# Optimization experiments

Hardware: AMD Instinct MI355X
Metric: run time of the kernel (lower is better)

Reference implementation:

```python
import jax, jax.numpy as jnp
import numpy as np

NUM_CLASSES = 91
NUM_ANCHORS = 3234
VAR_XY, VAR_WH = 0.1, 0.2
SCORE_THRESH = 0.05
NMS_THRESH = 0.5
PRE_NMS_TOPK = 200  # original default 400; reduced to bound the [C-1,K,K] IoU buffer
MAX_DET = 100
BATCH = 64


def _xyxy_to_cxcywh(b):
    wh = b[..., 2:] - b[..., :2]
    c = b[..., :2] + 0.5 * wh
    return jnp.concatenate([c, wh], axis=-1)


def _pairwise_iou(b):
    # b: [K,4] xyxy -> [K,K] IoU
    lt = jnp.maximum(b[:, None, :2], b[None, :, :2])
    rb = jnp.minimum(b[:, None, 2:], b[None, :, 2:])
    inter = jnp.prod(jnp.clip(rb - lt, 0.0), axis=-1)
    area = jnp.prod(jnp.clip(b[:, 2:] - b[:, :2], 0.0), axis=-1)
    union = area[:, None] + area[None, :] - inter
    return inter / jnp.maximum(union, 1e-9)


def _nms_keep(boxes):
    # boxes [K,4] already sorted by descending score; greedy NMS keep mask [K]
    K = boxes.shape[0]
    iou = _pairwise_iou(jax.lax.stop_gradient(boxes))
    idx = jnp.arange(K)

    def body(i, keep):
        suppress = keep[i] & (iou[i] > NMS_THRESH) & (idx > i)
        return keep & ~suppress

    return jax.lax.fori_loop(0, K, body, jnp.ones((K,), dtype=bool))


def setup_inputs() -> dict:
    key = jax.random.key(0)
    k1, k2, k3, k4 = jax.random.split(key, 4)
    cls_logits = jax.random.normal(k1, (BATCH, NUM_ANCHORS, NUM_CLASSES), dtype=jnp.float32)
    box_reg = jax.random.normal(k2, (BATCH, NUM_ANCHORS, 4), dtype=jnp.float32)
    # valid normalized anchor boxes in xyxy
    cxy = jax.random.uniform(k3, (NUM_ANCHORS, 2), minval=0.05, maxval=0.95)
    wh = jax.random.uniform(k4, (NUM_ANCHORS, 2), minval=0.02, maxval=0.4)
    priors = jnp.concatenate([cxy - wh / 2, cxy + wh / 2], axis=-1).astype(jnp.float32)
    return {"cls_logits": cls_logits, "box_reg": box_reg, "priors": priors}


def reference(cls_logits, box_reg, priors):
    probs = jax.nn.softmax(cls_logits, axis=-1)           # [B,A,C]
    pr_c = _xyxy_to_cxcywh(priors)                        # [A,4]

    def per_image(args):
        loc, p = args                                     # [A,4], [A,C]
        # _decode with variances (0.1, 0.2)
        xy = loc[:, :2] * VAR_XY * pr_c[:, 2:] + pr_c[:, :2]
        wh = jnp.exp(loc[:, 2:] * VAR_WH) * pr_c[:, 2:]
        boxes = jnp.concatenate([xy - wh / 2, xy + wh / 2], axis=-1)  # [A,4]

        scores_c = p[:, 1:].T                             # [C-1, A], skip background
        vals, idx = jax.lax.top_k(scores_c, PRE_NMS_TOPK)  # [C-1,K] sorted desc
        boxes_c = boxes[idx]                              # [C-1,K,4]
        keep = jax.vmap(_nms_keep)(boxes_c)               # [C-1,K]
        valid = vals > SCORE_THRESH
        fscores = jnp.where(keep & valid, vals, 0.0)      # masked-out dets scored 0
        labels = jnp.broadcast_to(
            jnp.arange(1, NUM_CLASSES, dtype=jnp.float32)[:, None], fscores.shape)

        flat_s = fscores.reshape(-1)
        flat_b = boxes_c.reshape(-1, 4)
        flat_l = labels.reshape(-1)
        top_s, top_i = jax.lax.top_k(flat_s, MAX_DET)     # global top-100 by score
        preds = jnp.concatenate(
            [flat_b[top_i], top_s[:, None], flat_l[top_i, None]], axis=-1)  # [100,6]
        return jnp.where(top_s[:, None] > 0, preds, 0.0)  # zero padding rows

    return jax.lax.map(per_image, (box_reg, probs))        # [B,100,6]
```

## Files before the change

kernel.cpp:

```cpp
#include <hip/hip_runtime.h>
#include <cstdint>

#define NCLS 91
#define NA   3234
#define NB   64
#define KTOP 200
#define CAP  128
#define MAXDET 100
#define NCM1 90
#define CAPI 8192
#define LCAP 256
#define NBIN 1024
#define BOFF 0x3D4C
#define FBUF 1024

typedef unsigned long long u64;
typedef unsigned int u32;


__device__ __forceinline__ u64 u64max(u64 a, u64 b) { return a > b ? a : b; }
__device__ __forceinline__ u64 u64min(u64 a, u64 b) { return a < b ? a : b; }

__device__ __forceinline__ u64 shfl_xor_u64(u64 v, int m) {
  int lo = __shfl_xor((int)(u32)v, m, 64);
  int hi = __shfl_xor((int)(u32)(v >> 32), m, 64);
  return ((u64)(u32)hi << 32) | (u32)lo;
}

template <int SLOTS>
__device__ __forceinline__ void bitonic_desc(u64* key, int t) {
  const int N = SLOTS * 64;
  for (int k = 2; k <= N; k <<= 1) {
    for (int j = k >> 1; j > 0; j >>= 1) {
      if (j >= 64) {
        int sj = j >> 6;
        #pragma unroll
        for (int s = 0; s < SLOTS; ++s) {
          int sp = s ^ sj;
          if (sp > s) {
            int e = s * 64 + t;
            bool up = ((e & k) == 0);
            u64 a = key[s], b = key[sp];
            u64 mx = u64max(a, b), mn = u64min(a, b);
            key[s]  = up ? mx : mn;
            key[sp] = up ? mn : mx;
          }
        }
      } else {
        #pragma unroll
        for (int s = 0; s < SLOTS; ++s) {
          int e = s * 64 + t;
          u64 p = shfl_xor_u64(key[s], j);
          bool up = ((e & k) == 0);
          bool lower = ((t & j) == 0);
          key[s] = (up == lower) ? u64max(key[s], p) : u64min(key[s], p);
        }
      }
    }
  }
}

__global__ __launch_bounds__(64) void prep_kernel(
    const float* __restrict__ logits, const float* __restrict__ box_reg,
    const float* __restrict__ priors, float* __restrict__ boxes,
    u64* __restrict__ cand, int* __restrict__ cnt) {
  __shared__ u64 lkey[LCAP];
  __shared__ unsigned short lbc[LCAP];
  __shared__ int lcnt;
  int t = threadIdx.x;
  if (t == 0) lcnt = 0;
  __syncthreads();

  int i = blockIdx.x * 64 + t;
  int b = i / NA, a = i - b * NA;

  float4 pr = ((const float4*)priors)[a];
  float pw = pr.z - pr.x, ph = pr.w - pr.y;
  float cx = pr.x + 0.5f * pw, cy = pr.y + 0.5f * ph;
  float4 lc = ((const float4*)box_reg)[i];
  float x = lc.x * 0.1f * pw + cx;
  float y = lc.y * 0.1f * ph + cy;
  float bw = expf(lc.z * 0.2f) * pw;
  float bh = expf(lc.w * 0.2f) * ph;
  float4 bxo;
  bxo.x = x - bw * 0.5f; bxo.y = y - bh * 0.5f;
  bxo.z = x + bw * 0.5f; bxo.w = y + bh * 0.5f;
  ((float4*)boxes)[i] = bxo;

  const float* lp = logits + (size_t)i * NCLS;
  int al = t & 3, nt = 3 - al;
  const float4* cv = (const float4*)(lp + al);

  float h0 = 0.f, h1 = 0.f, h2 = 0.f;
  if (al > 0) h0 = lp[0];
  if (al > 1) h1 = lp[1];
  if (al > 2) h2 = lp[2];
  float4 r[22];
  #pragma unroll
  for (int v = 0; v < 22; ++v) r[v] = cv[v];
  float q0 = 0.f, q1 = 0.f, q2 = 0.f;
  if (nt > 0) q0 = lp[al + 88];
  if (nt > 1) q1 = lp[al + 89];
  if (nt > 2) q2 = lp[al + 90];

  float m = -3.402823466e38f;
  if (al > 0) m = fmaxf(m, h0);
  if (al > 1) m = fmaxf(m, h1);
  if (al > 2) m = fmaxf(m, h2);
  #pragma unroll
  for (int v = 0; v < 22; ++v) {
    float4 q = r[v];
    m = fmaxf(m, fmaxf(fmaxf(q.x, q.y), fmaxf(q.z, q.w)));
  }
  if (nt > 0) m = fmaxf(m, q0);
  if (nt > 1) m = fmaxf(m, q1);
  if (nt > 2) m = fmaxf(m, q2);

  float ssum = 0.f;
  if (al > 0) ssum += expf(h0 - m);
  if (al > 1) ssum += expf(h1 - m);
  if (al > 2) ssum += expf(h2 - m);
  #pragma unroll
  for (int v = 0; v < 22; ++v) {
    float4 q = r[v];
    ssum += expf(q.x - m); ssum += expf(q.y - m);
    ssum += expf(q.z - m); ssum += expf(q.w - m);
  }
  if (nt > 0) ssum += expf(q0 - m);
  if (nt > 1) ssum += expf(q1 - m);
  if (nt > 2) ssum += expf(q2 - m);

  float lthr = logf(0.05f * ssum);
  u64 abits = (u64)(u32)(~a);
  int bb90 = b * NCM1;
  #define PUSH(L, CC) do { \
    float _d = (L) - m; \
    if (_d > lthr) { \
      float _e = expf(_d); \
      int _lp = atomicAdd(&lcnt, 1); \
      if (_lp < LCAP) { \
        lkey[_lp] = ((u64)__float_as_uint(_e / ssum) << 32) | abits; \
        lbc[_lp] = (unsigned short)(bb90 + (CC) - 1); \
      } \
    } \
  } while (0)

  if (al > 1) PUSH(h1, 1);
  if (al > 2) PUSH(h2, 2);
  #pragma unroll
  for (int v = 0; v < 22; ++v) {
    float4 q = r[v];
    int cb = al + 4 * v;
    if (v != 0 || al != 0) PUSH(q.x, cb);
    PUSH(q.y, cb + 1);
    PUSH(q.z, cb + 2);
    PUSH(q.w, cb + 3);
  }
  if (nt > 0) PUSH(q0, al + 88);
  if (nt > 1) PUSH(q1, al + 89);
  if (nt > 2) PUSH(q2, al + 90);
  #undef PUSH
  __syncthreads();

  int nL = lcnt; if (nL > LCAP) nL = LCAP;
  for (int j = t; j < nL; j += 64) {
    int bcv = lbc[j];
    int pos = atomicAdd(&cnt[bcv], 1);
    if (pos < CAP) cand[(size_t)bcv * CAP + pos] = lkey[j];
  }
}

__global__ __launch_bounds__(256) void sort_nms_kernel(
    const u64* __restrict__ cand, const int* __restrict__ cnt,
    const float* __restrict__ boxes,
    u64* __restrict__ img_keys, int* __restrict__ img_cnt) {
  __shared__ float4 sbx[4][CAP];
  __shared__ float sar[4][CAP];
  __shared__ u64 sm[4][CAP][2];
  int w = threadIdx.x >> 6;
  int t = threadIdx.x & 63;
  int bc = blockIdx.x * 4 + w;
  int b = bc / NCM1;
  int cm1 = bc - b * NCM1;

  int n = cnt[bc]; if (n > CAP) n = CAP;

  u64 key[2];
  #pragma unroll
  for (int s = 0; s < 2; ++s) {
    int e = s * 64 + t;
    key[s] = (e < n) ? cand[(size_t)bc * CAP + e] : 0ULL;
  }
  if (n <= 64) bitonic_desc<1>(key, t);
  else         bitonic_desc<2>(key, t);

  #pragma unroll
  for (int s = 0; s < 2; ++s) {
    int rr = s * 64 + t;
    if (rr < n) {
      int a = (int)(~(u32)key[s]);
      float4 bbx = ((const float4*)boxes)[b * NA + a];
      sbx[w][rr] = bbx;
      sar[w][rr] = fmaxf(bbx.z - bbx.x, 0.f) * fmaxf(bbx.w - bbx.y, 0.f);
    }
  }
  __syncthreads();

  #pragma unroll
  for (int T = 0; T < 2; ++T) {
    int rr = T * 64 + t;
    float4 bi; float ai = 0.f;
    bool act = (rr < n);
    if (act) { bi = sbx[w][rr]; ai = sar[w][rr]; }
    u64 m0 = 0, m1 = 0;
    for (int j = T * 64 + 1; j < n; ++j) {
      float4 bj = sbx[w][j];
      float aj = sar[w][j];
      if (act && j > rr) {
        float xx1 = fmaxf(bi.x, bj.x), yy1 = fmaxf(bi.y, bj.y);
        float xx2 = fminf(bi.z, bj.z), yy2 = fminf(bi.w, bj.w);
        float inter = fmaxf(xx2 - xx1, 0.f) * fmaxf(yy2 - yy1, 0.f);
        float iou = inter / fmaxf(ai + aj - inter, 1e-9f);
        if (iou > 0.5f) {
          if (j < 64) m0 |= 1ull << j;
          else        m1 |= 1ull << (j - 64);
        }
      }
    }
    if (act) { sm[w][rr][0] = m0; sm[w][rr][1] = m1; }
  }
  __syncthreads();

  u64 kp0 = ~0ull, kp1 = ~0ull;
  for (int i = 0; i < n; ++i) {
    u64 s0 = sm[w][i][0], s1 = sm[w][i][1];
    u64 kw = (i < 64) ? kp0 : kp1;
    u64 live = 0ull - ((kw >> (i & 63)) & 1ull);
    kp0 &= ~(s0 & live); kp1 &= ~(s1 & live);
  }

  auto rng = [](int mm, int wd) -> u64 {
    int c = mm - wd * 64;
    if (c <= 0) return 0ull;
    if (c >= 64) return ~0ull;
    return (1ull << c) - 1ull;
  };
  u64 k0 = kp0 & rng(n, 0), k1 = kp1 & rng(n, 1);
  int c0 = __popcll(k0), c1 = __popcll(k1);
  int tot = c0 + c1;
  int base = 0;
  if (t == 0 && tot) base = atomicAdd(&img_cnt[b], tot);
  base = __shfl(base, 0, 64);
  if (tot) {
    u64 lmlt = (1ull << t) - 1ull;
    u64 kws[2] = {k0, k1};
    int pres[2] = {0, c0};
    #pragma unroll
    for (int s = 0; s < 2; ++s) {
      int rr = s * 64 + t;
      if (rr < n && ((kws[s] >> t) & 1ull)) {
        int pos = base + pres[s] + __popcll(kws[s] & lmlt);
        if (pos < CAPI) {
          u32 sbits = (u32)(key[s] >> 32);
          int fidx = cm1 * KTOP + rr;
          int anch = (int)(~(u32)key[s]);
          img_keys[(size_t)b * CAPI + pos] =
              ((u64)sbits << 27) | ((u64)(u32)(0x7FFF - fidx) << 12) | (u64)(u32)anch;
        }
      }
    }
  }
}

__global__ __launch_bounds__(1024) void topdet_kernel(
    const u64* __restrict__ img_keys, const int* __restrict__ img_cnt,
    const float* __restrict__ boxes, float* __restrict__ out) {
  __shared__ int hist[NBIN];
  __shared__ u64 buf[FBUF];
  __shared__ int sh_nsel, sh_T;
  int b = blockIdx.x, t = threadIdx.x;
  int n = img_cnt[b]; if (n > CAPI) n = CAPI;

  for (int i = t; i < NBIN; i += 1024) hist[i] = 0;
  if (t == 0) { sh_nsel = 0; sh_T = 0; }
  __syncthreads();

  for (int i = t; i < n; i += 1024) {
    int bin = (int)(img_keys[(size_t)b * CAPI + i] >> 43) - BOFF;
    bin = bin < 0 ? 0 : (bin > NBIN - 1 ? NBIN - 1 : bin);
    atomicAdd(&hist[bin], 1);
  }
  __syncthreads();

  if (t < 64) {
    int hi = NBIN - 1 - (t << 4);
    int cs = 0;
    #pragma unroll
    for (int k = 0; k < 16; ++k) cs += hist[hi - k];
    int cum = cs;
    for (int d = 1; d < 64; d <<= 1) {
      int o = __shfl_up(cum, d, 64);
      if (t >= d) cum += o;
    }
    int pre = cum - cs;
    if (pre < MAXDET && cum >= MAXDET) {
      int acc = pre;
      for (int k = 0; k < 16; ++k) {
        acc += hist[hi - k];
        if (acc >= MAXDET) { sh_T = hi - k; break; }
      }
    }
  }
  __syncthreads();

  int T = sh_T;
  for (int i = t; i < n; i += 1024) {
    u64 key = img_keys[(size_t)b * CAPI + i];
    int bin = (int)(key >> 43) - BOFF;
    bin = bin < 0 ? 0 : (bin > NBIN - 1 ? NBIN - 1 : bin);
    if (bin >= T) {
      int pos = atomicAdd(&sh_nsel, 1);
      if (pos < FBUF) buf[pos] = key;
    }
  }
  __syncthreads();

  int ns = sh_nsel; if (ns > FBUF) ns = FBUF;

  if (ns <= 256) {
    if (t < 64) {
      u64 key[4];
      #pragma unroll
      for (int s = 0; s < 4; ++s) {
        int e = s * 64 + t;
        key[s] = (e < ns) ? buf[e] : 0ULL;
      }
      if (ns <= 128) bitonic_desc<2>(key, t);
      else           bitonic_desc<4>(key, t);
      buf[t] = key[0];
      if (t < 36) buf[64 + t] = key[1];
    }
    __syncthreads();
  } else {
    int npow = 1; while (npow < ns) npow <<= 1;
    for (int i = t; i < npow; i += 1024) if (i >= ns) buf[i] = 0ULL;
    __syncthreads();
    for (int k = 2; k <= npow; k <<= 1) {
      for (int j = k >> 1; j > 0; j >>= 1) {
        for (int i = t; i < npow; i += 1024) {
          int l = i ^ j;
          if (l > i) {
            u64 x0 = buf[i], x1 = buf[l];
            bool up = ((i & k) == 0);
            if (up ? (x0 < x1) : (x0 > x1)) { buf[i] = x1; buf[l] = x0; }
          }
        }
        __syncthreads();
      }
    }
  }

  if (t < MAXDET) {
    float* row = out + ((size_t)b * MAXDET + t) * 6;
    if (t < ns) {
      u64 key = buf[t];
      float vsc = __uint_as_float((u32)(key >> 27));
      int fidx = 0x7FFF - (int)((key >> 12) & 0x7FFF);
      int a = (int)(key & 0xFFF);
      float4 bb = ((const float4*)boxes)[b * NA + a];
      row[0] = bb.x; row[1] = bb.y; row[2] = bb.z; row[3] = bb.w;
      row[4] = vsc;
      row[5] = (float)(fidx / KTOP + 1);
    } else {
      row[0] = 0.f; row[1] = 0.f; row[2] = 0.f;
      row[3] = 0.f; row[4] = 0.f; row[5] = 0.f;
    }
  }
}

extern "C" void kernel_launch(void* const* d_in, const int* in_sizes, int n_in,
                              void* d_out, int out_size, void* d_ws, size_t ws_size,
                              hipStream_t stream) {
  const float* logits  = (const float*)d_in[0];
  const float* box_reg = (const float*)d_in[1];
  const float* priors  = (const float*)d_in[2];
  float* out = (float*)d_out;

  char* ws = (char*)d_ws;
  size_t off = 0;
  float* boxes = (float*)(ws + off);               off += (size_t)NB * NA * 4 * sizeof(float);
  u64* cand = (u64*)(ws + off);                    off += (size_t)NB * NCM1 * CAP * sizeof(u64);
  u64* img_keys = (u64*)(ws + off);                off += (size_t)NB * CAPI * sizeof(u64);
  int* cnt = (int*)(ws + off);                     off += (size_t)NB * NCM1 * sizeof(int);
  int* img_cnt = (int*)(ws + off);                 off += (size_t)NB * sizeof(int);
  (void)ws_size; (void)in_sizes; (void)n_in; (void)out_size;

  hipMemsetAsync(cnt, 0, (size_t)(NB * NCM1 + NB) * sizeof(int), stream);
  prep_kernel<<<NB * NA / 64, 64, 0, stream>>>(
      logits, box_reg, priors, boxes, cand, cnt);
  sort_nms_kernel<<<NB * NCM1 / 4, 256, 0, stream>>>(
      cand, cnt, boxes, img_keys, img_cnt);
  topdet_kernel<<<NB, 1024, 0, stream>>>(img_keys, img_cnt, boxes, out);
}
```

Measured before the change: 226.2 us.

## Process three slabs per block with software-pipelined register loads in prep kernel

The prep kernel now launches a third as many single-wave blocks, and each block handles three 64-row slabs. The next slab's logits are loaded into a second register buffer while the current slab computes, so global load latency overlaps with the softmax and push work. The __syncthreads calls are replaced by lgkmcnt waits, which is valid only because each block is a single 64-thread wave. The extra register buffer roughly doubles register pressure and may lower occupancy.

Measured after the change: 294.0 us. +30.0%, slower.

```diff
diff --git a/kernel.cpp b/kernel.cpp
--- a/kernel.cpp
+++ b/kernel.cpp
@@ -13,6 +13,8 @@
 #define NBIN 1024
 #define BOFF 0x3D4C
 #define FBUF 1024
+#define NSLAB 3234
+#define PGRID 1078
 
 typedef unsigned long long u64;
 typedef unsigned int u32;
@@ -60,75 +62,81 @@
   }
 }
 
-__global__ __launch_bounds__(64) void prep_kernel(
+
+struct RowBuf {
+  float4 r[22];
+  float h0, h1, h2, q0, q1, q2;
+  float4 pr, lc;
+};
+
+__device__ __forceinline__ void load_slab(
+    RowBuf& B, int s, int t,
     const float* __restrict__ logits, const float* __restrict__ box_reg,
-    const float* __restrict__ priors, float* __restrict__ boxes,
-    u64* __restrict__ cand, int* __restrict__ cnt) {
-  __shared__ u64 lkey[LCAP];
-  __shared__ unsigned short lbc[LCAP];
-  __shared__ int lcnt;
-  int t = threadIdx.x;
-  if (t == 0) lcnt = 0;
-  __syncthreads();
-
-  int i = blockIdx.x * 64 + t;
+    const float* __restrict__ priors) {
+  int i = s * 64 + t;
   int b = i / NA, a = i - b * NA;
-
-  float4 pr = ((const float4*)priors)[a];
-  float pw = pr.z - pr.x, ph = pr.w - pr.y;
-  float cx = pr.x + 0.5f * pw, cy = pr.y + 0.5f * ph;
-  float4 lc = ((const float4*)box_reg)[i];
-  float x = lc.x * 0.1f * pw + cx;
-  float y = lc.y * 0.1f * ph + cy;
-  float bw = expf(lc.z * 0.2f) * pw;
-  float bh = expf(lc.w * 0.2f) * ph;
+  B.pr = ((const float4*)priors)[a];
+  B.lc = ((const float4*)box_reg)[i];
+  const float* lp = logits + (size_t)i * NCLS;
+  int al = t & 3, nt = 3 - al;
+  const float4* cv = (const float4*)(lp + al);
+  B.h0 = 0.f; B.h1 = 0.f; B.h2 = 0.f;
+  if (al > 0) B.h0 = lp[0];
+  if (al > 1) B.h1 = lp[1];
+  if (al > 2) B.h2 = lp[2];
+  #pragma unroll
+  for (int v = 0; v < 22; ++v) B.r[v] = cv[v];
+  B.q0 = 0.f; B.q1 = 0.f; B.q2 = 0.f;
+  if (nt > 0) B.q0 = lp[al + 88];
+  if (nt > 1) B.q1 = lp[al + 89];
+  if (nt > 2) B.q2 = lp[al + 90];
+}
+
+__device__ __forceinline__ void compute_slab(
+    RowBuf& B, int s, int t,
+    u64* lkey, unsigned short* lbc, int* plcnt,
+    float* __restrict__ boxes, u64* __restrict__ cand, int* __restrict__ cnt) {
+  int i = s * 64 + t;
+  int b = i / NA, a = i - b * NA;
+  int al = t & 3, nt = 3 - al;
+
+  float pw = B.pr.z - B.pr.x, phh = B.pr.w - B.pr.y;
+  float cx = B.pr.x + 0.5f * pw, cy = B.pr.y + 0.5f * phh;
+  float x = B.lc.x * 0.1f * pw + cx;
+  float y = B.lc.y * 0.1f * phh + cy;
+  float bw = expf(B.lc.z * 0.2f) * pw;
+  float bh = expf(B.lc.w * 0.2f) * phh;
   float4 bxo;
   bxo.x = x - bw * 0.5f; bxo.y = y - bh * 0.5f;
   bxo.z = x + bw * 0.5f; bxo.w = y + bh * 0.5f;
   ((float4*)boxes)[i] = bxo;
 
-  const float* lp = logits + (size_t)i * NCLS;
-  int al = t & 3, nt = 3 - al;
-  const float4* cv = (const float4*)(lp + al);
-
-  float h0 = 0.f, h1 = 0.f, h2 = 0.f;
-  if (al > 0) h0 = lp[0];
-  if (al > 1) h1 = lp[1];
-  if (al > 2) h2 = lp[2];
-  float4 r[22];
-  #pragma unroll
-  for (int v = 0; v < 22; ++v) r[v] = cv[v];
-  float q0 = 0.f, q1 = 0.f, q2 = 0.f;
-  if (nt > 0) q0 = lp[al + 88];
-  if (nt > 1) q1 = lp[al + 89];
-  if (nt > 2) q2 = lp[al + 90];
-
   float m = -3.402823466e38f;
-  if (al > 0) m = fmaxf(m, h0);
-  if (al > 1) m = fmaxf(m, h1);
-  if (al > 2) m = fmaxf(m, h2);
+  if (al > 0) m = fmaxf(m, B.h0);
+  if (al > 1) m = fmaxf(m, B.h1);
+  if (al > 2) m = fmaxf(m, B.h2);
   #pragma unroll
   for (int v = 0; v < 22; ++v) {
-    float4 q = r[v];
+    float4 q = B.r[v];
     m = fmaxf(m, fmaxf(fmaxf(q.x, q.y), fmaxf(q.z, q.w)));
   }
-  if (nt > 0) m = fmaxf(m, q0);
-  if (nt > 1) m = fmaxf(m, q1);
-  if (nt > 2) m = fmaxf(m, q2);
+  if (nt > 0) m = fmaxf(m, B.q0);
+  if (nt > 1) m = fmaxf(m, B.q1);
+  if (nt > 2) m = fmaxf(m, B.q2);
 
   float ssum = 0.f;
-  if (al > 0) ssum += expf(h0 - m);
-  if (al > 1) ssum += expf(h1 - m);
-  if (al > 2) ssum += expf(h2 - m);
+  if (al > 0) ssum += expf(B.h0 - m);
+  if (al > 1) ssum += expf(B.h1 - m);
+  if (al > 2) ssum += expf(B.h2 - m);
   #pragma unroll
   for (int v = 0; v < 22; ++v) {
-    float4 q = r[v];
+    float4 q = B.r[v];
     ssum += expf(q.x - m); ssum += expf(q.y - m);
     ssum += expf(q.z - m); ssum += expf(q.w - m);
   }
-  if (nt > 0) ssum += expf(q0 - m);
-  if (nt > 1) ssum += expf(q1 - m);
-  if (nt > 2) ssum += expf(q2 - m);
+  if (nt > 0) ssum += expf(B.q0 - m);
+  if (nt > 1) ssum += expf(B.q1 - m);
+  if (nt > 2) ssum += expf(B.q2 - m);
 
   float lthr = logf(0.05f * ssum);
   u64 abits = (u64)(u32)(~a);
@@ -137,7 +145,7 @@
     float _d = (L) - m; \
     if (_d > lthr) { \
       float _e = expf(_d); \
-      int _lp = atomicAdd(&lcnt, 1); \
+      int _lp = atomicAdd(plcnt, 1); \
       if (_lp < LCAP) { \
         lkey[_lp] = ((u64)__float_as_uint(_e / ssum) << 32) | abits; \
         lbc[_lp] = (unsigned short)(bb90 + (CC) - 1); \
@@ -145,29 +153,50 @@
     } \
   } while (0)
 
-  if (al > 1) PUSH(h1, 1);
-  if (al > 2) PUSH(h2, 2);
+  if (al > 1) PUSH(B.h1, 1);
+  if (al > 2) PUSH(B.h2, 2);
   #pragma unroll
   for (int v = 0; v < 22; ++v) {
-    float4 q = r[v];
+    float4 q = B.r[v];
     int cb = al + 4 * v;
     if (v != 0 || al != 0) PUSH(q.x, cb);
     PUSH(q.y, cb + 1);
     PUSH(q.z, cb + 2);
     PUSH(q.w, cb + 3);
   }
-  if (nt > 0) PUSH(q0, al + 88);
-  if (nt > 1) PUSH(q1, al + 89);
-  if (nt > 2) PUSH(q2, al + 90);
+  if (nt > 0) PUSH(B.q0, al + 88);
+  if (nt > 1) PUSH(B.q1, al + 89);
+  if (nt > 2) PUSH(B.q2, al + 90);
   #undef PUSH
-  __syncthreads();
-
-  int nL = lcnt; if (nL > LCAP) nL = LCAP;
+
+  asm volatile("s_waitcnt lgkmcnt(0)" ::: "memory");
+  int nL = *plcnt; if (nL > LCAP) nL = LCAP;
   for (int j = t; j < nL; j += 64) {
     int bcv = lbc[j];
     int pos = atomicAdd(&cnt[bcv], 1);
     if (pos < CAP) cand[(size_t)bcv * CAP + pos] = lkey[j];
   }
+}
+
+__global__ __launch_bounds__(64) void prep_kernel(
+    const float* __restrict__ logits, const float* __restrict__ box_reg,
+    const float* __restrict__ priors, float* __restrict__ boxes,
+    u64* __restrict__ cand, int* __restrict__ cnt) {
+  __shared__ u64 lkey3[3][LCAP];
+  __shared__ unsigned short lbc3[3][LCAP];
+  __shared__ int lcnt3[3];
+  int t = threadIdx.x;
+  if (t < 3) lcnt3[t] = 0;
+  asm volatile("s_waitcnt lgkmcnt(0)" ::: "memory");
+
+  RowBuf A, Bb;
+  int s0 = blockIdx.x, s1 = s0 + PGRID, s2 = s1 + PGRID;
+  load_slab(A, s0, t, logits, box_reg, priors);
+  load_slab(Bb, s1, t, logits, box_reg, priors);
+  compute_slab(A, s0, t, lkey3[0], lbc3[0], &lcnt3[0], boxes, cand, cnt);
+  load_slab(A, s2, t, logits, box_reg, priors);
+  compute_slab(Bb, s1, t, lkey3[1], lbc3[1], &lcnt3[1], boxes, cand, cnt);
+  compute_slab(A, s2, t, lkey3[2], lbc3[2], &lcnt3[2], boxes, cand, cnt);
 }
 
 __global__ __launch_bounds__(256) void sort_nms_kernel(
@@ -396,7 +425,7 @@
   (void)ws_size; (void)in_sizes; (void)n_in; (void)out_size;
 
   hipMemsetAsync(cnt, 0, (size_t)(NB * NCM1 + NB) * sizeof(int), stream);
-  prep_kernel<<<NB * NA / 64, 64, 0, stream>>>(
+  prep_kernel<<<PGRID, 64, 0, stream>>>(
       logits, box_reg, priors, boxes, cand, cnt);
   sort_nms_kernel<<<NB * NCM1 / 4, 256, 0, stream>>>(
       cand, cnt, boxes, img_keys, img_cnt);
```

## Split each anchor's softmax across two lanes and drop block barriers in prep

Applied to the files above, without the earlier changes.

The prep kernel now assigns two lanes per anchor, each loading and processing about half of the 91 class logits. The lanes combine their max and exp-sum through shuffles, and the grid doubles to 6468 blocks. The exp sum is made serial across the two lanes so the floating-point summation order matches the earlier single-lane code. The block-level __syncthreads are replaced with s_waitcnt plus sched_barrier, which is valid only because the block is a single 64-lane wavefront. The aim is lower register pressure and more parallelism in the softmax/threshold stage, at the cost of extra shuffles and a serialized FOLD.

Result: no change. 225.9 us (-0.1%).

```diff
diff --git a/kernel.cpp b/kernel.cpp
--- a/kernel.cpp
+++ b/kernel.cpp
@@ -13,6 +13,7 @@
 #define NBIN 1024
 #define BOFF 0x3D4C
 #define FBUF 1024
+#define PBLK 6468
 
 typedef unsigned long long u64;
 typedef unsigned int u32;
@@ -69,66 +70,100 @@
   __shared__ int lcnt;
   int t = threadIdx.x;
   if (t == 0) lcnt = 0;
-  __syncthreads();
-
-  int i = blockIdx.x * 64 + t;
+  asm volatile("s_waitcnt lgkmcnt(0)" ::: "memory");
+  __builtin_amdgcn_sched_barrier(0);
+
+  int half = t & 1;
+  int rloc = t >> 1;
+  int i = blockIdx.x * 32 + rloc;
   int b = i / NA, a = i - b * NA;
 
-  float4 pr = ((const float4*)priors)[a];
-  float pw = pr.z - pr.x, ph = pr.w - pr.y;
-  float cx = pr.x + 0.5f * pw, cy = pr.y + 0.5f * ph;
-  float4 lc = ((const float4*)box_reg)[i];
-  float x = lc.x * 0.1f * pw + cx;
-  float y = lc.y * 0.1f * ph + cy;
-  float bw = expf(lc.z * 0.2f) * pw;
-  float bh = expf(lc.w * 0.2f) * ph;
-  float4 bxo;
-  bxo.x = x - bw * 0.5f; bxo.y = y - bh * 0.5f;
-  bxo.z = x + bw * 0.5f; bxo.w = y + bh * 0.5f;
-  ((float4*)boxes)[i] = bxo;
-
+  int F0   = half ? 45 : 0;
+  int cntf = half ? 46 : 45;
   const float* lp = logits + (size_t)i * NCLS;
-  int al = t & 3, nt = 3 - al;
-  const float4* cv = (const float4*)(lp + al);
-
-  float h0 = 0.f, h1 = 0.f, h2 = 0.f;
-  if (al > 0) h0 = lp[0];
-  if (al > 1) h1 = lp[1];
-  if (al > 2) h2 = lp[2];
-  float4 r[22];
-  #pragma unroll
-  for (int v = 0; v < 22; ++v) r[v] = cv[v];
-  float q0 = 0.f, q1 = 0.f, q2 = 0.f;
-  if (nt > 0) q0 = lp[al + 88];
-  if (nt > 1) q1 = lp[al + 89];
-  if (nt > 2) q2 = lp[al + 90];
+  const float* base = lp + F0;
+  int g0 = (int)(((u32)(i * NCLS + F0)) & 3u);
+  int lead = (4 - g0) & 3;
+  int rem = cntf - lead;
+  int n4 = rem >> 2;
+  int tail = rem & 3;
+
+  float lv0 = 0.f, lv1 = 0.f, lv2 = 0.f;
+  if (lead > 0) lv0 = base[0];
+  if (lead > 1) lv1 = base[1];
+  if (lead > 2) lv2 = base[2];
+  const float4* cv = (const float4*)(base + lead);
+  float4 r[11];
+  #pragma unroll
+  for (int v = 0; v < 10; ++v) r[v] = cv[v];
+  r[10] = make_float4(0.f, 0.f, 0.f, 0.f);
+  if (n4 > 10) r[10] = cv[10];
+  int toff = lead + 4 * n4;
+  float tv0 = 0.f, tv1 = 0.f, tv2 = 0.f;
+  if (tail > 0) tv0 = base[toff];
+  if (tail > 1) tv1 = base[toff + 1];
+  if (tail > 2) tv2 = base[toff + 2];
+
+  if (!half) {
+    float4 pr = ((const float4*)priors)[a];
+    float pw = pr.z - pr.x, ph = pr.w - pr.y;
+    float cx = pr.x + 0.5f * pw, cy = pr.y + 0.5f * ph;
+    float4 lc = ((const float4*)box_reg)[i];
+    float x = lc.x * 0.1f * pw + cx;
+    float y = lc.y * 0.1f * ph + cy;
+    float bw = expf(lc.z * 0.2f) * pw;
+    float bh = expf(lc.w * 0.2f) * ph;
+    float4 bxo;
+    bxo.x = x - bw * 0.5f; bxo.y = y - bh * 0.5f;
+    bxo.z = x + bw * 0.5f; bxo.w = y + bh * 0.5f;
+    ((float4*)boxes)[i] = bxo;
+  }
 
   float m = -3.402823466e38f;
-  if (al > 0) m = fmaxf(m, h0);
-  if (al > 1) m = fmaxf(m, h1);
-  if (al > 2) m = fmaxf(m, h2);
-  #pragma unroll
-  for (int v = 0; v < 22; ++v) {
+  if (lead > 0) m = fmaxf(m, lv0);
+  if (lead > 1) m = fmaxf(m, lv1);
+  if (lead > 2) m = fmaxf(m, lv2);
+  #pragma unroll
+  for (int v = 0; v < 10; ++v) {
     float4 q = r[v];
     m = fmaxf(m, fmaxf(fmaxf(q.x, q.y), fmaxf(q.z, q.w)));
   }
-  if (nt > 0) m = fmaxf(m, q0);
-  if (nt > 1) m = fmaxf(m, q1);
-  if (nt > 2) m = fmaxf(m, q2);
-
-  float ssum = 0.f;
-  if (al > 0) ssum += expf(h0 - m);
-  if (al > 1) ssum += expf(h1 - m);
-  if (al > 2) ssum += expf(h2 - m);
-  #pragma unroll
-  for (int v = 0; v < 22; ++v) {
-    float4 q = r[v];
-    ssum += expf(q.x - m); ssum += expf(q.y - m);
-    ssum += expf(q.z - m); ssum += expf(q.w - m);
-  }
-  if (nt > 0) ssum += expf(q0 - m);
-  if (nt > 1) ssum += expf(q1 - m);
-  if (nt > 2) ssum += expf(q2 - m);
+  if (n4 > 10) {
+    float4 q = r[10];
+    m = fmaxf(m, fmaxf(fmaxf(q.x, q.y), fmaxf(q.z, q.w)));
+  }
+  if (tail > 0) m = fmaxf(m, tv0);
+  if (tail > 1) m = fmaxf(m, tv1);
+  if (tail > 2) m = fmaxf(m, tv2);
+  m = fmaxf(m, __shfl_xor(m, 1, 64));
+
+  auto FOLD = [&](float s) -> float {
+    if (lead > 0) s += expf(lv0 - m);
+    if (lead > 1) s += expf(lv1 - m);
+    if (lead > 2) s += expf(lv2 - m);
+    #pragma unroll
+    for (int v = 0; v < 10; ++v) {
+      float4 q = r[v];
+      s += expf(q.x - m); s += expf(q.y - m);
+      s += expf(q.z - m); s += expf(q.w - m);
+    }
+    if (n4 > 10) {
+      float4 q = r[10];
+      s += expf(q.x - m); s += expf(q.y - m);
+      s += expf(q.z - m); s += expf(q.w - m);
+    }
+    if (tail > 0) s += expf(tv0 - m);
+    if (tail > 1) s += expf(tv1 - m);
+    if (tail > 2) s += expf(tv2 - m);
+    return s;
+  };
+
+  float s = 0.f;
+  if (!half) s = FOLD(0.f);
+  float s_recv = __shfl_xor(s, 1, 64);
+  if (half) s = FOLD(s_recv);
+  float fin = __shfl_xor(s, 1, 64);
+  float ssum = half ? s : fin;
 
   float lthr = logf(0.05f * ssum);
   u64 abits = (u64)(u32)(~a);
@@ -145,23 +180,36 @@
     } \
   } while (0)
 
-  if (al > 1) PUSH(h1, 1);
-  if (al > 2) PUSH(h2, 2);
-  #pragma unroll
-  for (int v = 0; v < 22; ++v) {
+  if (lead > 0 && F0 != 0) PUSH(lv0, F0);
+  if (lead > 1) PUSH(lv1, F0 + 1);
+  if (lead > 2) PUSH(lv2, F0 + 2);
+  {
+    int c0 = F0 + lead;
+    float4 q = r[0];
+    if (c0 != 0) PUSH(q.x, c0);
+    PUSH(q.y, c0 + 1); PUSH(q.z, c0 + 2); PUSH(q.w, c0 + 3);
+  }
+  #pragma unroll
+  for (int v = 1; v < 10; ++v) {
     float4 q = r[v];
-    int cb = al + 4 * v;
-    if (v != 0 || al != 0) PUSH(q.x, cb);
-    PUSH(q.y, cb + 1);
-    PUSH(q.z, cb + 2);
-    PUSH(q.w, cb + 3);
-  }
-  if (nt > 0) PUSH(q0, al + 88);
-  if (nt > 1) PUSH(q1, al + 89);
-  if (nt > 2) PUSH(q2, al + 90);
+    int cb = F0 + lead + 4 * v;
+    PUSH(q.x, cb); PUSH(q.y, cb + 1); PUSH(q.z, cb + 2); PUSH(q.w, cb + 3);
+  }
+  if (n4 > 10) {
+    float4 q = r[10];
+    int cb = F0 + lead + 40;
+    PUSH(q.x, cb); PUSH(q.y, cb + 1); PUSH(q.z, cb + 2); PUSH(q.w, cb + 3);
+  }
+  {
+    int cb = F0 + toff;
+    if (tail > 0) PUSH(tv0, cb);
+    if (tail > 1) PUSH(tv1, cb + 1);
+    if (tail > 2) PUSH(tv2, cb + 2);
+  }
   #undef PUSH
-  __syncthreads();
-
+
+  asm volatile("s_waitcnt lgkmcnt(0)" ::: "memory");
+  __builtin_amdgcn_sched_barrier(0);
   int nL = lcnt; if (nL > LCAP) nL = LCAP;
   for (int j = t; j < nL; j += 64) {
     int bcv = lbc[j];
@@ -396,7 +444,7 @@
   (void)ws_size; (void)in_sizes; (void)n_in; (void)out_size;
 
   hipMemsetAsync(cnt, 0, (size_t)(NB * NCM1 + NB) * sizeof(int), stream);
-  prep_kernel<<<NB * NA / 64, 64, 0, stream>>>(
+  prep_kernel<<<PBLK, 64, 0, stream>>>(
       logits, box_reg, priors, boxes, cand, cnt);
   sort_nms_kernel<<<NB * NCM1 / 4, 256, 0, stream>>>(
       cand, cnt, boxes, img_keys, img_cnt);
```
